# Kernel optimization log

Measured on AMD Instinct MI355X. Metric: run time of the kernel, lower is better.

## Reference

```python
import jax, jax.numpy as jnp
import numpy as np

B, L, T = 8, 1024, 10
K = 1.0                 # soft_sign sharpness (config.k)
S = float(np.log(9.0))  # self.s
W_PEN = 1.0             # self.w


def soft_sign(x):
    return jax.nn.sigmoid(2.0 * K * x)


def mlp2(f, W1, b1, W2, b2):
    # pointwise 2-layer MLP with ReLU after each layer; output dim 1 -> squeeze
    h = jax.nn.relu(jnp.einsum('...i,oi->...o', f, W1) + b1)
    return jax.nn.relu(jnp.einsum('...i,oi->...o', h, W2) + b2)[..., 0]


def setup_inputs() -> dict:
    key = jax.random.key(0)
    ks = jax.random.split(key, 16)
    u = jax.random.normal(ks[0], (B, L, L), jnp.float32)
    x = jax.random.uniform(ks[1], (B, L, 4), jnp.float32)
    p = lambda k, s: (jax.random.normal(k, s, jnp.float32) * 0.5)
    return dict(
        u=u, x=x, timesteps=T,
        aW1=p(ks[2], (T, 3, 3)), ab1=p(ks[3], (T, 3)), aW2=p(ks[4], (T, 1, 3)), ab2=p(ks[5], (T, 1)),
        rW1=p(ks[6], (T, 3, 3)), rb1=p(ks[7], (T, 3)), rW2=p(ks[8], (T, 1, 3)), rb2=p(ks[9], (T, 1)),
        lW1=p(ks[10], (T, 3, 2)), lb1=p(ks[11], (T, 3)), lW2=p(ks[12], (T, 1, 3)), lb2=p(ks[13], (T, 1)),
    )


def reference(u, x, timesteps, aW1, ab1, aW2, ab2, rW1, rb1, rW2, rb2, lW1, lb1, lW2, lb2):
    # constraint matrix m: sum of symmetrized outer products of base channels
    ba, bu, bc, bg = x[:, :, 0], x[:, :, 1], x[:, :, 2], x[:, :, 3]
    def sym_outer(p, q):
        o = jnp.einsum('bi,bj->bij', p, q)
        return o + o.swapaxes(-1, -2)
    m = sym_outer(ba, bu) + sym_outer(bc, bg) + sym_outer(bu, bg)

    def contact(ah):
        aa = ah * ah
        return (aa + aa.swapaxes(-1, -2)) * 0.5 * m

    uu = soft_sign(u - S) * u
    a_hat = jax.nn.sigmoid(uu) * soft_sign(uu - S)
    a = contact(a_hat)
    lmbd = W_PEN * jax.nn.relu(jnp.sum(a, -1) - 1.0)

    outs = []
    for t in range(timesteps):  # fixed unroll, distinct params per step
        grad_a = -uu * 0.5 + (lmbd * soft_sign(jnp.sum(a, -1) - 1.0))[..., None]
        grad = a_hat * m * (grad_a + grad_a.swapaxes(-1, -2))
        feats = jnp.stack([a_hat, grad, uu], -1)  # [B,L,L,3]
        ah_new = mlp2(feats, aW1[t], ab1[t], aW2[t], ab2[t])
        rho = mlp2(feats, rW1[t], rb1[t], rW2[t], rb2[t])
        ah_new = jnp.clip(jax.nn.relu(jnp.abs(ah_new) - rho), -1.0, 1.0)
        a = contact(ah_new)
        lg = jax.nn.relu(jnp.sum(a, -1) - 1.0)
        lmbd = mlp2(jnp.stack([lmbd, lg], -1), lW1[t], lb1[t], lW2[t], lb2[t])
        a_hat = ah_new
        outs.append(a)
    return jnp.stack(outs)  # [T,B,L,L] == a_t_list[1:]
```

## Files before the change

kernel.cpp:

```cpp
#include <hip/hip_runtime.h>
#include <hip/hip_bf16.h>

#define BB 8
#define LL 1024
#define TT 10
#define TILE 64
#define NTILE (LL/TILE)
#define NPAIR (NTILE*(NTILE+1)/2)
#define SPAD 65
#define S_CONST 2.1972245773362196f

typedef __hip_bfloat16 bf16;

static __device__ __forceinline__ float sigm(float v) {
    return 1.0f / (1.0f + __expf(-v));
}

static __device__ __forceinline__ void pair_from_idx(int p, int& I, int& J) {
    int i = 0;
    while (p >= NTILE - i) { p -= NTILE - i; i++; }
    I = i; J = i + p;
}

static __device__ __forceinline__ float compute_m(const float* xI, const float* xJ, int r, int c) {
    float bai = xI[0*TILE + r], bui = xI[1*TILE + r], bci = xI[2*TILE + r], bgi = xI[3*TILE + r];
    float baj = xJ[0*TILE + c], buj = xJ[1*TILE + c], bcj = xJ[2*TILE + c], bgj = xJ[3*TILE + c];
    return bai*buj + baj*bui + bci*bgj + bcj*bgi + bui*bgj + buj*bgi;
}

static __device__ __forceinline__ float mlp3(float f0, float f1, float f2, const float* w) {
    float h0 = fmaxf(w[0]*f0 + w[1]*f1 + w[2]*f2 + w[9],  0.0f);
    float h1 = fmaxf(w[3]*f0 + w[4]*f1 + w[5]*f2 + w[10], 0.0f);
    float h2 = fmaxf(w[6]*f0 + w[7]*f1 + w[8]*f2 + w[11], 0.0f);
    return fmaxf(w[12]*h0 + w[13]*h1 + w[14]*h2 + w[15], 0.0f);
}

static __device__ __forceinline__ float ahnew_calc(float ah, float grad, float uuv, const float* w) {
    float va = mlp3(ah, grad, uuv, w);
    float vr = mlp3(ah, grad, uuv, w + 16);
    float v = fmaxf(fabsf(va) - vr, 0.0f);
    return fminf(v, 1.0f);
}

__global__ void k_prep(const float* __restrict__ u,
                       bf16* __restrict__ uu, bf16* __restrict__ ahat) {
    const long long N = (long long)BB * LL * LL;
    for (long long i = (long long)blockIdx.x * blockDim.x + threadIdx.x; i < N;
         i += (long long)gridDim.x * blockDim.x) {
        float uv  = u[i];
        float uuv = sigm(2.0f * (uv - S_CONST)) * uv;
        float ah  = sigm(uuv) * sigm(2.0f * (uuv - S_CONST));
        uu[i]   = __float2bfloat16(uuv);
        ahat[i] = __float2bfloat16(ah);
    }
}

__global__ __launch_bounds__(256) void k_rs0(const bf16* __restrict__ ahat,
                                             const float* __restrict__ x,
                                             float* __restrict__ rs) {
    __shared__ float stB[TILE * SPAD];
    __shared__ float xI[4 * TILE], xJ[4 * TILE];
    __shared__ float rsI[TILE], rsJ[TILE];

    int b = blockIdx.x / NPAIR, p = blockIdx.x % NPAIR;
    int I, J; pair_from_idx(p, I, J);
    int Ib = I * TILE, Jb = J * TILE;
    bool diag = (I == J);
    int tid = threadIdx.x, c = tid & 63, rg = tid >> 6;

    { int row = tid >> 2, k = tid & 3;
      xI[k*TILE + row] = x[((size_t)b*LL + Ib + row)*4 + k];
      xJ[k*TILE + row] = x[((size_t)b*LL + Jb + row)*4 + k]; }
    if (tid < TILE) { rsI[tid] = 0.0f; rsJ[tid] = 0.0f; }

    float ahv[16];
    size_t baseIJ = ((size_t)b*LL + Ib)*LL + Jb;
    #pragma unroll
    for (int k = 0; k < 16; k++)
        ahv[k] = __bfloat162float(ahat[baseIJ + (size_t)(rg + 4*k)*LL + c]);

    size_t baseJI = ((size_t)b*LL + Jb)*LL + Ib;
    #pragma unroll
    for (int k = 0; k < 16; k++) {
        int xr = rg + 4*k;
        stB[xr*SPAD + c] = __bfloat162float(ahat[baseJI + (size_t)xr*LL + c]);
    }
    __syncthreads();

    float rsJ_th = 0.0f;
    #pragma unroll
    for (int k = 0; k < 16; k++) {
        int r = rg + 4*k;
        float ah_ij = ahv[k];
        float ah_ji = stB[c*SPAD + r];
        float m = compute_m(xI, xJ, r, c);
        float a_val = 0.5f * (ah_ij*ah_ij + ah_ji*ah_ji) * m;
        float s = a_val;
        for (int off = 32; off; off >>= 1) s += __shfl_down(s, off, 64);
        if (c == 0) rsI[r] += s;
        if (!diag) rsJ_th += a_val;
    }
    if (!diag) atomicAdd(&rsJ[c], rsJ_th);
    __syncthreads();
    if (tid < TILE) atomicAdd(&rs[b*LL + Ib + tid], rsI[tid]);
    else if (!diag && tid < 2*TILE) atomicAdd(&rs[b*LL + Jb + (tid - TILE)], rsJ[tid - TILE]);
}

__global__ void k_rows_init(const float* __restrict__ rs0, float* __restrict__ lmbd,
                            float* __restrict__ ls, float* __restrict__ rs_other) {
    int i = blockIdx.x * blockDim.x + threadIdx.x;
    if (i < BB*LL) {
        float rsv = rs0[i];
        float l = fmaxf(rsv - 1.0f, 0.0f);
        lmbd[i] = l;
        ls[i] = l * sigm(2.0f * (rsv - 1.0f));
        rs_other[i] = 0.0f;
    }
}

__global__ __launch_bounds__(256) void k_step(
        const bf16* __restrict__ uu, bf16* __restrict__ ahat,
        const float* __restrict__ x,
        const float* __restrict__ ls, float* __restrict__ rs_next,
        const float* __restrict__ aW1, const float* __restrict__ ab1,
        const float* __restrict__ aW2, const float* __restrict__ ab2,
        const float* __restrict__ rW1, const float* __restrict__ rb1,
        const float* __restrict__ rW2, const float* __restrict__ rb2,
        float* __restrict__ out, int t) {
    __shared__ float stA[TILE * SPAD];
    __shared__ float stB[TILE * SPAD];
    __shared__ float xI[4 * TILE], xJ[4 * TILE];
    __shared__ float lsI[TILE], lsJ[TILE];
    __shared__ float w[32];
    __shared__ float rsI[TILE], rsJ[TILE];

    int b = blockIdx.x / NPAIR, p = blockIdx.x % NPAIR;
    int I, J; pair_from_idx(p, I, J);
    int Ib = I * TILE, Jb = J * TILE;
    bool diag = (I == J);
    int tid = threadIdx.x, c = tid & 63, rg = tid >> 6;

    float uuv[16], ahv[16];
    size_t baseIJ = ((size_t)b*LL + Ib)*LL + Jb;
    #pragma unroll
    for (int k = 0; k < 16; k++) {
        size_t idx = baseIJ + (size_t)(rg + 4*k)*LL + c;
        uuv[k] = __bfloat162float(uu[idx]);
        ahv[k] = __bfloat162float(ahat[idx]);
    }

    if (tid < 32) {
        float v;
        if      (tid <  9) v = aW1[t*9 + tid];
        else if (tid < 12) v = ab1[t*3 + (tid-9)];
        else if (tid < 15) v = aW2[t*3 + (tid-12)];
        else if (tid < 16) v = ab2[t];
        else if (tid < 25) v = rW1[t*9 + (tid-16)];
        else if (tid < 28) v = rb1[t*3 + (tid-25)];
        else if (tid < 31) v = rW2[t*3 + (tid-28)];
        else               v = rb2[t];
        w[tid] = v;
    }
    { int row = tid >> 2, k = tid & 3;
      xI[k*TILE + row] = x[((size_t)b*LL + Ib + row)*4 + k];
      xJ[k*TILE + row] = x[((size_t)b*LL + Jb + row)*4 + k]; }
    if (tid < TILE) {
        lsI[tid] = ls[b*LL + Ib + tid];
        lsJ[tid] = ls[b*LL + Jb + tid];
        rsI[tid] = 0.0f; rsJ[tid] = 0.0f;
    }
    size_t baseJI = ((size_t)b*LL + Jb)*LL + Ib;
    #pragma unroll
    for (int k = 0; k < 16; k++) {
        int xr = rg + 4*k;
        stA[xr*SPAD + c] = __bfloat162float(uu[baseJI + (size_t)xr*LL + c]);
        stB[xr*SPAD + c] = __bfloat162float(ahat[baseJI + (size_t)xr*LL + c]);
    }
    __syncthreads();

    size_t outBase = (((size_t)t*BB + b) * LL) * LL;
    float rsJ_th = 0.0f;
    #pragma unroll
    for (int k = 0; k < 16; k++) {
        int r = rg + 4*k;
        size_t idxIJ = baseIJ + (size_t)r*LL + c;
        float uu_ij = uuv[k];
        float ah_ij = ahv[k];
        float uu_ji = stA[c*SPAD + r];
        float ah_ji = stB[c*SPAD + r];
        float m = compute_m(xI, xJ, r, c);
        float gsum = -0.5f * (uu_ij + uu_ji) + lsI[r] + lsJ[c];
        float an_ij = ahnew_calc(ah_ij, ah_ij * m * gsum, uu_ij, w);
        float an_ji = ahnew_calc(ah_ji, ah_ji * m * gsum, uu_ji, w);
        float a_val = 0.5f * (an_ij*an_ij + an_ji*an_ji) * m;

        ahat[idxIJ] = __float2bfloat16(an_ij);
        __builtin_nontemporal_store(a_val, &out[outBase + (size_t)(Ib + r)*LL + (Jb + c)]);

        float s = a_val;
        for (int off = 32; off; off >>= 1) s += __shfl_down(s, off, 64);
        if (c == 0) rsI[r] += s;

        if (!diag) {
            stA[c*SPAD + r] = a_val;
            stB[c*SPAD + r] = an_ji;
            rsJ_th += a_val;
        }
    }
    if (!diag) atomicAdd(&rsJ[c], rsJ_th);
    __syncthreads();
    if (!diag) {
        #pragma unroll
        for (int k = 0; k < 16; k++) {
            int xr = rg + 4*k;
            ahat[baseJI + (size_t)xr*LL + c] = __float2bfloat16(stB[xr*SPAD + c]);
            __builtin_nontemporal_store(stA[xr*SPAD + c],
                                        &out[outBase + (size_t)(Jb + xr)*LL + (Ib + c)]);
        }
    }
    if (tid < TILE) atomicAdd(&rs_next[b*LL + Ib + tid], rsI[tid]);
    else if (!diag && tid < 2*TILE) atomicAdd(&rs_next[b*LL + Jb + (tid - TILE)], rsJ[tid - TILE]);
}

__global__ void k_rows_step(const float* __restrict__ rs_new, float* lmbd, float* __restrict__ ls,
                            float* __restrict__ rs_zero,
                            const float* __restrict__ lW1, const float* __restrict__ lb1,
                            const float* __restrict__ lW2, const float* __restrict__ lb2,
                            int t) {
    int i = blockIdx.x * blockDim.x + threadIdx.x;
    if (i < BB*LL) {
        float rsv = rs_new[i];
        float lg = fmaxf(rsv - 1.0f, 0.0f);
        float l0 = lmbd[i];
        float w0 = lW1[t*6 + 0], w1 = lW1[t*6 + 1];
        float w2 = lW1[t*6 + 2], w3 = lW1[t*6 + 3];
        float w4 = lW1[t*6 + 4], w5 = lW1[t*6 + 5];
        float b0 = lb1[t*3 + 0], b1 = lb1[t*3 + 1];
        float b2 = lb1[t*3 + 2];
        float v0 = lW2[t*3 + 0], v1 = lW2[t*3 + 1];
        float v2 = lW2[t*3 + 2];
        float c2 = lb2[t];
        float h0 = fmaxf(w0*l0 + w1*lg + b0, 0.0f);
        float h1 = fmaxf(w2*l0 + w3*lg + b1, 0.0f);
        float h2 = fmaxf(w4*l0 + w5*lg + b2, 0.0f);
        float ln = fmaxf(v0*h0 + v1*h1 + v2*h2 + c2, 0.0f);
        lmbd[i] = ln;
        ls[i] = ln * sigm(2.0f * (rsv - 1.0f));
        rs_zero[i] = 0.0f;
    }
}

extern "C" void kernel_launch(void* const* d_in, const int* in_sizes, int n_in,
                              void* d_out, int out_size, void* d_ws, size_t ws_size,
                              hipStream_t stream) {
    const float* u   = (const float*)d_in[0];
    const float* x   = (const float*)d_in[1];
    const float* aW1 = (const float*)d_in[3];
    const float* ab1 = (const float*)d_in[4];
    const float* aW2 = (const float*)d_in[5];
    const float* ab2 = (const float*)d_in[6];
    const float* rW1 = (const float*)d_in[7];
    const float* rb1 = (const float*)d_in[8];
    const float* rW2 = (const float*)d_in[9];
    const float* rb2 = (const float*)d_in[10];
    const float* lW1 = (const float*)d_in[11];
    const float* lb1 = (const float*)d_in[12];
    const float* lW2 = (const float*)d_in[13];
    const float* lb2 = (const float*)d_in[14];
    float* out = (float*)d_out;

    char* ws = (char*)d_ws;
    size_t matB2 = (size_t)BB * LL * LL * sizeof(bf16);
    bf16* uu   = (bf16*)ws;
    bf16* ahat = (bf16*)(ws + matB2);
    float* rs0  = (float*)(ws + 2 * matB2);
    float* rs1  = rs0 + BB*LL;
    float* lmbd = rs1 + BB*LL;
    float* ls   = lmbd + BB*LL;

    hipMemsetAsync(rs0, 0, BB*LL*sizeof(float), stream);
    hipLaunchKernelGGL(k_prep, dim3(2048), dim3(256), 0, stream, u, uu, ahat);
    hipLaunchKernelGGL(k_rs0, dim3(BB*NPAIR), dim3(256), 0, stream, ahat, x, rs0);
    hipLaunchKernelGGL(k_rows_init, dim3((BB*LL)/256), dim3(256), 0, stream, rs0, lmbd, ls, rs1);

    float* rsb[2] = {rs0, rs1};
    for (int t = 0; t < TT; ++t) {
        hipLaunchKernelGGL(k_step, dim3(BB*NPAIR), dim3(256), 0, stream,
                           uu, ahat, x, ls, rsb[(t+1)&1],
                           aW1, ab1, aW2, ab2, rW1, rb1, rW2, rb2, out, t);
        hipLaunchKernelGGL(k_rows_step, dim3((BB*LL)/256), dim3(256), 0, stream,
                           rsb[(t+1)&1], lmbd, ls, rsb[t&1], lW1, lb1, lW2, lb2, t);
    }
}
```

Measured before the change: 663.0 us.

## Fuse prep/rowsum/row kernels into step kernels and interleave uu/ahat storage

Merges the elementwise prep and the initial row-sum into one init kernel, and folds the per-row lambda MLP into the start of each step kernel, so the separate small row kernels and their launches go away. uu and ahat are packed into one 32-bit word per element, so each step reads and writes a single array. The shuffle-based row reductions become a shared-memory column sum, and the m formula is factored to need fewer multiplies. Each block now recomputes lambda for its own rows redundantly, and a per-step row-sum buffer replaces ping-pong zeroing.

```diff
diff --git a/kernel.cpp b/kernel.cpp
--- a/kernel.cpp
+++ b/kernel.cpp
@@ -16,16 +16,27 @@
     return 1.0f / (1.0f + __expf(-v));
 }
 
+static __device__ __forceinline__ unsigned short f2bf(float v) {
+    bf16 h = __float2bfloat16(v);
+    unsigned short b; __builtin_memcpy(&b, &h, 2); return b;
+}
+static __device__ __forceinline__ float lo2f(unsigned int v) {
+    return __uint_as_float(v << 16);
+}
+static __device__ __forceinline__ float hi2f(unsigned int v) {
+    return __uint_as_float(v & 0xffff0000u);
+}
+static __device__ __forceinline__ unsigned int pk2(float uu, float ah) {
+    return (unsigned int)f2bf(uu) | ((unsigned int)f2bf(ah) << 16);
+}
+static __device__ __forceinline__ unsigned int pk_rt(float uu_exact, float ah) {
+    return (__float_as_uint(uu_exact) >> 16) | ((unsigned int)f2bf(ah) << 16);
+}
+
 static __device__ __forceinline__ void pair_from_idx(int p, int& I, int& J) {
     int i = 0;
     while (p >= NTILE - i) { p -= NTILE - i; i++; }
     I = i; J = i + p;
-}
-
-static __device__ __forceinline__ float compute_m(const float* xI, const float* xJ, int r, int c) {
-    float bai = xI[0*TILE + r], bui = xI[1*TILE + r], bci = xI[2*TILE + r], bgi = xI[3*TILE + r];
-    float baj = xJ[0*TILE + c], buj = xJ[1*TILE + c], bcj = xJ[2*TILE + c], bgj = xJ[3*TILE + c];
-    return bai*buj + baj*bui + bci*bgj + bcj*bgi + bui*bgj + buj*bgi;
 }
 
 static __device__ __forceinline__ float mlp3(float f0, float f1, float f2, const float* w) {
@@ -42,22 +53,11 @@
     return fminf(v, 1.0f);
 }
 
-__global__ void k_prep(const float* __restrict__ u,
-                       bf16* __restrict__ uu, bf16* __restrict__ ahat) {
-    const long long N = (long long)BB * LL * LL;
-    for (long long i = (long long)blockIdx.x * blockDim.x + threadIdx.x; i < N;
-         i += (long long)gridDim.x * blockDim.x) {
-        float uv  = u[i];
-        float uuv = sigm(2.0f * (uv - S_CONST)) * uv;
-        float ah  = sigm(uuv) * sigm(2.0f * (uuv - S_CONST));
-        uu[i]   = __float2bfloat16(uuv);
-        ahat[i] = __float2bfloat16(ah);
-    }
-}
-
-__global__ __launch_bounds__(256) void k_rs0(const bf16* __restrict__ ahat,
-                                             const float* __restrict__ x,
-                                             float* __restrict__ rs) {
+__global__ __launch_bounds__(256) void k_init(const float* __restrict__ u,
+                                              const float* __restrict__ x,
+                                              unsigned int* __restrict__ st,
+                                              float* __restrict__ rs0) {
+    __shared__ float stA[TILE * SPAD];
     __shared__ float stB[TILE * SPAD];
     __shared__ float xI[4 * TILE], xJ[4 * TILE];
     __shared__ float rsI[TILE], rsJ[TILE];
@@ -68,64 +68,74 @@
     bool diag = (I == J);
     int tid = threadIdx.x, c = tid & 63, rg = tid >> 6;
 
-    { int row = tid >> 2, k = tid & 3;
-      xI[k*TILE + row] = x[((size_t)b*LL + Ib + row)*4 + k];
-      xJ[k*TILE + row] = x[((size_t)b*LL + Jb + row)*4 + k]; }
+    { int row = tid >> 2, k2 = tid & 3;
+      xI[k2*TILE + row] = x[((size_t)b*LL + Ib + row)*4 + k2];
+      xJ[k2*TILE + row] = x[((size_t)b*LL + Jb + row)*4 + k2]; }
     if (tid < TILE) { rsI[tid] = 0.0f; rsJ[tid] = 0.0f; }
 
     float ahv[16];
     size_t baseIJ = ((size_t)b*LL + Ib)*LL + Jb;
     #pragma unroll
-    for (int k = 0; k < 16; k++)
-        ahv[k] = __bfloat162float(ahat[baseIJ + (size_t)(rg + 4*k)*LL + c]);
-
+    for (int k = 0; k < 16; k++) {
+        size_t idx = baseIJ + (size_t)(rg + 4*k)*LL + c;
+        float uv  = u[idx];
+        float uuv = sigm(2.0f*(uv - S_CONST)) * uv;
+        float ah  = sigm(uuv) * sigm(2.0f*(uuv - S_CONST));
+        unsigned int pkd = pk2(uuv, ah);
+        st[idx] = pkd;
+        ahv[k] = hi2f(pkd);
+    }
     size_t baseJI = ((size_t)b*LL + Jb)*LL + Ib;
     #pragma unroll
     for (int k = 0; k < 16; k++) {
         int xr = rg + 4*k;
-        stB[xr*SPAD + c] = __bfloat162float(ahat[baseJI + (size_t)xr*LL + c]);
-    }
-    __syncthreads();
-
+        size_t idx = baseJI + (size_t)xr*LL + c;
+        float uv  = u[idx];
+        float uuv = sigm(2.0f*(uv - S_CONST)) * uv;
+        float ah  = sigm(uuv) * sigm(2.0f*(uuv - S_CONST));
+        unsigned int pkd = pk2(uuv, ah);
+        if (!diag) st[idx] = pkd;
+        stB[xr*SPAD + c] = hi2f(pkd);
+    }
+    __syncthreads();
+
+    float buj = xJ[1*TILE + c], bgj = xJ[3*TILE + c];
+    float s1j = xJ[0*TILE + c] + bgj;
+    float s2j = xJ[2*TILE + c] + buj;
     float rsJ_th = 0.0f;
     #pragma unroll
     for (int k = 0; k < 16; k++) {
         int r = rg + 4*k;
         float ah_ij = ahv[k];
         float ah_ji = stB[c*SPAD + r];
-        float m = compute_m(xI, xJ, r, c);
-        float a_val = 0.5f * (ah_ij*ah_ij + ah_ji*ah_ji) * m;
-        float s = a_val;
-        for (int off = 32; off; off >>= 1) s += __shfl_down(s, off, 64);
-        if (c == 0) rsI[r] += s;
-        if (!diag) rsJ_th += a_val;
+        float m = xI[0*TILE + r]*buj + xI[2*TILE + r]*bgj
+                + xI[1*TILE + r]*s1j + xI[3*TILE + r]*s2j;
+        float a0 = 0.5f * (ah_ij*ah_ij + ah_ji*ah_ji) * m;
+        stA[c*SPAD + r] = a0;
+        rsJ_th += a0;
     }
     if (!diag) atomicAdd(&rsJ[c], rsJ_th);
     __syncthreads();
-    if (tid < TILE) atomicAdd(&rs[b*LL + Ib + tid], rsI[tid]);
-    else if (!diag && tid < 2*TILE) atomicAdd(&rs[b*LL + Jb + (tid - TILE)], rsJ[tid - TILE]);
-}
-
-__global__ void k_rows_init(const float* __restrict__ rs0, float* __restrict__ lmbd,
-                            float* __restrict__ ls, float* __restrict__ rs_other) {
-    int i = blockIdx.x * blockDim.x + threadIdx.x;
-    if (i < BB*LL) {
-        float rsv = rs0[i];
-        float l = fmaxf(rsv - 1.0f, 0.0f);
-        lmbd[i] = l;
-        ls[i] = l * sigm(2.0f * (rsv - 1.0f));
-        rs_other[i] = 0.0f;
-    }
+    { int r = tid & 63, g = tid >> 6;
+      float s = 0.0f;
+      #pragma unroll
+      for (int q = 0; q < 16; q++) s += stA[(g*16 + q)*SPAD + r];
+      atomicAdd(&rsI[r], s); }
+    __syncthreads();
+    if (tid < TILE) atomicAdd(&rs0[b*LL + Ib + tid], rsI[tid]);
+    else if (!diag && tid < 2*TILE) atomicAdd(&rs0[b*LL + Jb + (tid - TILE)], rsJ[tid - TILE]);
 }
 
 __global__ __launch_bounds__(256) void k_step(
-        const bf16* __restrict__ uu, bf16* __restrict__ ahat,
-        const float* __restrict__ x,
-        const float* __restrict__ ls, float* __restrict__ rs_next,
+        unsigned int* __restrict__ st, const float* __restrict__ x,
+        const float* __restrict__ rs_cur, float* __restrict__ rs_next,
+        const float* __restrict__ lmbd_prev, float* __restrict__ lmbd_next,
         const float* __restrict__ aW1, const float* __restrict__ ab1,
         const float* __restrict__ aW2, const float* __restrict__ ab2,
         const float* __restrict__ rW1, const float* __restrict__ rb1,
         const float* __restrict__ rW2, const float* __restrict__ rb2,
+        const float* __restrict__ lw1, const float* __restrict__ lb1_,
+        const float* __restrict__ lw2, const float* __restrict__ lb2_,
         float* __restrict__ out, int t) {
     __shared__ float stA[TILE * SPAD];
     __shared__ float stB[TILE * SPAD];
@@ -144,9 +154,9 @@
     size_t baseIJ = ((size_t)b*LL + Ib)*LL + Jb;
     #pragma unroll
     for (int k = 0; k < 16; k++) {
-        size_t idx = baseIJ + (size_t)(rg + 4*k)*LL + c;
-        uuv[k] = __bfloat162float(uu[idx]);
-        ahv[k] = __bfloat162float(ahat[idx]);
+        unsigned int v = st[baseIJ + (size_t)(rg + 4*k)*LL + c];
+        uuv[k] = lo2f(v);
+        ahv[k] = hi2f(v);
     }
 
     if (tid < 32) {
@@ -161,23 +171,45 @@
         else               v = rb2[t];
         w[tid] = v;
     }
-    { int row = tid >> 2, k = tid & 3;
-      xI[k*TILE + row] = x[((size_t)b*LL + Ib + row)*4 + k];
-      xJ[k*TILE + row] = x[((size_t)b*LL + Jb + row)*4 + k]; }
-    if (tid < TILE) {
-        lsI[tid] = ls[b*LL + Ib + tid];
-        lsJ[tid] = ls[b*LL + Jb + tid];
-        rsI[tid] = 0.0f; rsJ[tid] = 0.0f;
+    { int row = tid >> 2, k2 = tid & 3;
+      xI[k2*TILE + row] = x[((size_t)b*LL + Ib + row)*4 + k2];
+      xJ[k2*TILE + row] = x[((size_t)b*LL + Jb + row)*4 + k2]; }
+    if (tid < TILE) { rsI[tid] = 0.0f; rsJ[tid] = 0.0f; }
+    if (tid < 128) {
+        int row = (tid < 64) ? (Ib + tid) : (Jb + tid - 64);
+        float rsv = rs_cur[b*LL + row];
+        float lg  = fmaxf(rsv - 1.0f, 0.0f);
+        float lam;
+        if (t == 0) {
+            lam = lg;
+        } else {
+            float l0 = lmbd_prev[b*LL + row];
+            float h0 = fmaxf(lw1[0]*l0 + lw1[1]*lg + lb1_[0], 0.0f);
+            float h1 = fmaxf(lw1[2]*l0 + lw1[3]*lg + lb1_[1], 0.0f);
+            float h2 = fmaxf(lw1[4]*l0 + lw1[5]*lg + lb1_[2], 0.0f);
+            lam = fmaxf(lw2[0]*h0 + lw2[1]*h1 + lw2[2]*h2 + lb2_[0], 0.0f);
+        }
+        float lsv = lam * sigm(2.0f*(rsv - 1.0f));
+        if (tid < 64) {
+            lsI[tid] = lsv;
+            if (diag) lmbd_next[b*LL + row] = lam;
+        } else {
+            lsJ[tid - 64] = lsv;
+        }
     }
     size_t baseJI = ((size_t)b*LL + Jb)*LL + Ib;
     #pragma unroll
     for (int k = 0; k < 16; k++) {
         int xr = rg + 4*k;
-        stA[xr*SPAD + c] = __bfloat162float(uu[baseJI + (size_t)xr*LL + c]);
-        stB[xr*SPAD + c] = __bfloat162float(ahat[baseJI + (size_t)xr*LL + c]);
-    }
-    __syncthreads();
-
+        unsigned int v = st[baseJI + (size_t)xr*LL + c];
+        stA[xr*SPAD + c] = lo2f(v);
+        stB[xr*SPAD + c] = hi2f(v);
+    }
+    __syncthreads();
+
+    float buj = xJ[1*TILE + c], bgj = xJ[3*TILE + c];
+    float s1j = xJ[0*TILE + c] + bgj;
+    float s2j = xJ[2*TILE + c] + buj;
     size_t outBase = (((size_t)t*BB + b) * LL) * LL;
     float rsJ_th = 0.0f;
     #pragma unroll
@@ -188,24 +220,19 @@
         float ah_ij = ahv[k];
         float uu_ji = stA[c*SPAD + r];
         float ah_ji = stB[c*SPAD + r];
-        float m = compute_m(xI, xJ, r, c);
+        float m = xI[0*TILE + r]*buj + xI[2*TILE + r]*bgj
+                + xI[1*TILE + r]*s1j + xI[3*TILE + r]*s2j;
         float gsum = -0.5f * (uu_ij + uu_ji) + lsI[r] + lsJ[c];
         float an_ij = ahnew_calc(ah_ij, ah_ij * m * gsum, uu_ij, w);
         float an_ji = ahnew_calc(ah_ji, ah_ji * m * gsum, uu_ji, w);
         float a_val = 0.5f * (an_ij*an_ij + an_ji*an_ji) * m;
 
-        ahat[idxIJ] = __float2bfloat16(an_ij);
+        st[idxIJ] = pk_rt(uu_ij, an_ij);
         __builtin_nontemporal_store(a_val, &out[outBase + (size_t)(Ib + r)*LL + (Jb + c)]);
 
-        float s = a_val;
-        for (int off = 32; off; off >>= 1) s += __shfl_down(s, off, 64);
-        if (c == 0) rsI[r] += s;
-
-        if (!diag) {
-            stA[c*SPAD + r] = a_val;
-            stB[c*SPAD + r] = an_ji;
-            rsJ_th += a_val;
-        }
+        stA[c*SPAD + r] = a_val;
+        stB[c*SPAD + r] = __uint_as_float(pk_rt(uu_ji, an_ji));
+        rsJ_th += a_val;
     }
     if (!diag) atomicAdd(&rsJ[c], rsJ_th);
     __syncthreads();
@@ -213,40 +240,20 @@
         #pragma unroll
         for (int k = 0; k < 16; k++) {
             int xr = rg + 4*k;
-            ahat[baseJI + (size_t)xr*LL + c] = __float2bfloat16(stB[xr*SPAD + c]);
+            st[baseJI + (size_t)xr*LL + c] = __float_as_uint(stB[xr*SPAD + c]);
             __builtin_nontemporal_store(stA[xr*SPAD + c],
                                         &out[outBase + (size_t)(Jb + xr)*LL + (Ib + c)]);
         }
     }
-    if (tid < TILE) atomicAdd(&rs_next[b*LL + Ib + tid], rsI[tid]);
-    else if (!diag && tid < 2*TILE) atomicAdd(&rs_next[b*LL + Jb + (tid - TILE)], rsJ[tid - TILE]);
-}
-
-__global__ void k_rows_step(const float* __restrict__ rs_new, float* lmbd, float* __restrict__ ls,
-                            float* __restrict__ rs_zero,
-                            const float* __restrict__ lW1, const float* __restrict__ lb1,
-                            const float* __restrict__ lW2, const float* __restrict__ lb2,
-                            int t) {
-    int i = blockIdx.x * blockDim.x + threadIdx.x;
-    if (i < BB*LL) {
-        float rsv = rs_new[i];
-        float lg = fmaxf(rsv - 1.0f, 0.0f);
-        float l0 = lmbd[i];
-        float w0 = lW1[t*6 + 0], w1 = lW1[t*6 + 1];
-        float w2 = lW1[t*6 + 2], w3 = lW1[t*6 + 3];
-        float w4 = lW1[t*6 + 4], w5 = lW1[t*6 + 5];
-        float b0 = lb1[t*3 + 0], b1 = lb1[t*3 + 1];
-        float b2 = lb1[t*3 + 2];
-        float v0 = lW2[t*3 + 0], v1 = lW2[t*3 + 1];
-        float v2 = lW2[t*3 + 2];
-        float c2 = lb2[t];
-        float h0 = fmaxf(w0*l0 + w1*lg + b0, 0.0f);
-        float h1 = fmaxf(w2*l0 + w3*lg + b1, 0.0f);
-        float h2 = fmaxf(w4*l0 + w5*lg + b2, 0.0f);
-        float ln = fmaxf(v0*h0 + v1*h1 + v2*h2 + c2, 0.0f);
-        lmbd[i] = ln;
-        ls[i] = ln * sigm(2.0f * (rsv - 1.0f));
-        rs_zero[i] = 0.0f;
+    if (t != TT-1) {
+        int r = tid & 63, g = tid >> 6;
+        float s = 0.0f;
+        #pragma unroll
+        for (int q = 0; q < 16; q++) s += stA[(g*16 + q)*SPAD + r];
+        atomicAdd(&rsI[r], s);
+        __syncthreads();
+        if (tid < TILE) atomicAdd(&rs_next[b*LL + Ib + tid], rsI[tid]);
+        else if (!diag && tid < 2*TILE) atomicAdd(&rs_next[b*LL + Jb + (tid - TILE)], rsJ[tid - TILE]);
     }
 }
 
@@ -270,25 +277,25 @@
     float* out = (float*)d_out;
 
     char* ws = (char*)d_ws;
-    size_t matB2 = (size_t)BB * LL * LL * sizeof(bf16);
-    bf16* uu   = (bf16*)ws;
-    bf16* ahat = (bf16*)(ws + matB2);
-    float* rs0  = (float*)(ws + 2 * matB2);
-    float* rs1  = rs0 + BB*LL;
-    float* lmbd = rs1 + BB*LL;
-    float* ls   = lmbd + BB*LL;
-
-    hipMemsetAsync(rs0, 0, BB*LL*sizeof(float), stream);
-    hipLaunchKernelGGL(k_prep, dim3(2048), dim3(256), 0, stream, u, uu, ahat);
-    hipLaunchKernelGGL(k_rs0, dim3(BB*NPAIR), dim3(256), 0, stream, ahat, x, rs0);
-    hipLaunchKernelGGL(k_rows_init, dim3((BB*LL)/256), dim3(256), 0, stream, rs0, lmbd, ls, rs1);
-
-    float* rsb[2] = {rs0, rs1};
+    size_t stBytes = (size_t)BB * LL * LL * sizeof(unsigned int);
+    unsigned int* st = (unsigned int*)ws;
+    float* rs    = (float*)(ws + stBytes);
+    float* lmbdA = rs + (size_t)TT * BB * LL;
+    float* lmbdB = lmbdA + BB * LL;
+
+    hipMemsetAsync(rs, 0, (size_t)TT * BB * LL * sizeof(float), stream);
+    hipLaunchKernelGGL(k_init, dim3(BB*NPAIR), dim3(256), 0, stream, u, x, st, rs);
+
     for (int t = 0; t < TT; ++t) {
+        float* lnext = (t & 1) ? lmbdB : lmbdA;
+        float* lprev = (t & 1) ? lmbdA : lmbdB;
+        const float* rs_cur = rs + (size_t)t * BB * LL;
+        float* rs_nextp = (t < TT-1) ? (rs + (size_t)(t+1) * BB * LL) : rs;
+        int toff = (t > 0) ? (t - 1) : 0;
         hipLaunchKernelGGL(k_step, dim3(BB*NPAIR), dim3(256), 0, stream,
-                           uu, ahat, x, ls, rsb[(t+1)&1],
-                           aW1, ab1, aW2, ab2, rW1, rb1, rW2, rb2, out, t);
-        hipLaunchKernelGGL(k_rows_step, dim3((BB*LL)/256), dim3(256), 0, stream,
-                           rsb[(t+1)&1], lmbd, ls, rsb[t&1], lW1, lb1, lW2, lb2, t);
-    }
-}
+                           st, x, rs_cur, rs_nextp, lprev, lnext,
+                           aW1, ab1, aW2, ab2, rW1, rb1, rW2, rb2,
+                           lW1 + toff*6, lb1 + toff*3, lW2 + toff*3, lb2 + toff,
+                           out, t);
+    }
+}
```

New measurement: 591.2 us. 10.8% less time.
